# Kernel tuning notes

Measured on AMD Instinct MI355X. Metric: run time of the kernel, lower is better.

## Reference

```python
import jax, jax.numpy as jnp
import numpy as np

B, T, D, ACT, H = 4096, 128, 64, 2, 64

def setup_inputs() -> dict:
    key = jax.random.key(0)
    ks = jax.random.split(key, 8)
    s = 1.0 / np.sqrt(H)
    return {
        "s0": jax.random.normal(ks[0], (B, D), jnp.float32),
        "a": jax.random.normal(ks[1], (B, T, ACT), jnp.float32),
        "w_ih": jax.random.uniform(ks[2], (3 * H, D + ACT), jnp.float32, -s, s),
        "w_hh": jax.random.uniform(ks[3], (3 * H, H), jnp.float32, -s, s),
        "b_ih": jax.random.uniform(ks[4], (3 * H,), jnp.float32, -s, s),
        "b_hh": jax.random.uniform(ks[5], (3 * H,), jnp.float32, -s, s),
        "w_out": jax.random.uniform(ks[6], (D, H), jnp.float32, -s, s),
        "b_out": jax.random.uniform(ks[7], (D,), jnp.float32, -s, s),
    }

def reference(s0, a, w_ih, w_hh, b_ih, b_hh, w_out, b_out):
    # PyTorch GRUCell convention: gates ordered (r, z, n)
    h0 = jnp.zeros((s0.shape[0], w_hh.shape[1]), s0.dtype)

    def step(carry, a_t):
        h, s = carry
        x = jnp.concatenate([s, a_t], axis=-1)              # [B, D+ACT]
        gi = x @ w_ih.T + b_ih                              # [B, 3H]
        gh = h @ w_hh.T + b_hh                              # [B, 3H]
        i_r, i_z, i_n = jnp.split(gi, 3, axis=-1)
        h_r, h_z, h_n = jnp.split(gh, 3, axis=-1)
        r = jax.nn.sigmoid(i_r + h_r)
        z = jax.nn.sigmoid(i_z + h_z)
        n = jnp.tanh(i_n + r * h_n)
        h_new = (1.0 - z) * n + z * h
        s_new = h_new @ w_out.T + b_out                     # [B, D]
        return (h_new, s_new), s_new

    a_tbd = jnp.swapaxes(a, 0, 1)                           # [T, B, ACT]
    _, outs = jax.lax.scan(step, (h0, s0), a_tbd)           # outs: [T, B, D]
    return jnp.swapaxes(outs, 0, 1)                         # [B, T, D]
```

## Files before the change

### kernel.cpp

```cpp
#include <hip/hip_runtime.h>
#include <hip/hip_bf16.h>

typedef __attribute__((ext_vector_type(8))) short bf16x8;
typedef __attribute__((ext_vector_type(4))) float f32x4;
typedef __attribute__((ext_vector_type(2))) float f32x2;

typedef bf16x8 bf16x8_a __attribute__((may_alias));
typedef f32x4  f32x4_a  __attribute__((may_alias));
typedef f32x2  f32x2_a  __attribute__((may_alias));
typedef unsigned short u16a __attribute__((may_alias));
typedef unsigned int u32;

__device__ __forceinline__ float fexp2(float x) {
  float r; asm("v_exp_f32 %0, %1" : "=v"(r) : "v"(x)); return r;
}
__device__ __forceinline__ float frcp(float x) {
  float r; asm("v_rcp_f32 %0, %1" : "=v"(r) : "v"(x)); return r;
}
__device__ __forceinline__ float sigf(float x) {
  return frcp(1.f + fexp2(x * -1.44269504f));
}
__device__ __forceinline__ float tanhf_(float x) {
  return 1.f - 2.f * frcp(1.f + fexp2(x * 2.88539008f));
}
__device__ __forceinline__ u32 cvtpk(float lo, float hi) {
  u32 r; asm("v_cvt_pk_bf16_f32 %0, %1, %2" : "=v"(r) : "v"(lo), "v"(hi)); return r;
}

#define LDS_WG   0
#define LDS_HB   24576
#define LDS_SIZE 28672

__device__ __forceinline__ void stbf(char* smem, int byteoff, float v) {
  union { __hip_bfloat16 b; unsigned short u; } cv;
  cv.b = __float2bfloat16(v);
  *(u16a*)(smem + byteoff) = cv.u;
}
__device__ __forceinline__ void st16(char* smem, int byteoff, unsigned short v) {
  *(u16a*)(smem + byteoff) = v;
}

__device__ __forceinline__ bf16x8 packf8(const float* v) {
  bf16x8 r;
  #pragma unroll
  for (int j = 0; j < 8; ++j) {
    union { __hip_bfloat16 b; short u; } cv;
    cv.b = __float2bfloat16(v[j]);
    r[j] = cv.u;
  }
  return r;
}

__device__ __forceinline__ void xbar() {
  asm volatile("s_waitcnt lgkmcnt(0)\n\ts_barrier" ::: "memory");
}

__global__ __launch_bounds__(256, 1)
void gru_fused(const float* __restrict__ s0, const float* __restrict__ a,
               const float* __restrict__ w_ih, const float* __restrict__ w_hh,
               const float* __restrict__ b_ih, const float* __restrict__ b_hh,
               const float* __restrict__ w_out, const float* __restrict__ b_out,
               float* __restrict__ out)
{
  __shared__ __align__(16) char smem[LDS_SIZE];
  const int tid = threadIdx.x;
  const int l = tid & 63;
  const int w = tid >> 6;
  const int c = l & 15;
  const int g = l >> 4;
  const int b0 = blockIdx.x * 16;
  const int swzc = (c & 7) << 4;

  for (int idx = tid; idx < 16 * 64; idx += 256) {
    int r = idx >> 6, k = idx & 63;
    stbf(smem, LDS_HB + r * 128 + ((k * 2) ^ ((r & 7) << 4)), s0[(b0 + r) * 64 + k]);
  }

  bf16x8 bwo[4][2];
  #pragma unroll
  for (int i = 0; i < 4; ++i) {
    #pragma unroll
    for (int ks = 0; ks < 2; ++ks) {
      float tv[8];
      #pragma unroll
      for (int j = 0; j < 8; ++j)
        tv[j] = w_out[(ks * 32 + g * 8 + j) * 64 + c + 16 * i];
      bwo[i][ks] = packf8(tv);
    }
  }
  #pragma unroll
  for (int rr = 0; rr < 3; ++rr) {
    int rt = w + 4 * rr;
    bf16x8 wsa[2];
    #pragma unroll
    for (int ks = 0; ks < 2; ++ks) {
      float tv[8];
      #pragma unroll
      for (int u = 0; u < 4; ++u) {
        f32x2 t2 = *(const f32x2_a*)(w_ih + (16 * rt + c) * 66 + ks * 32 + g * 8 + 2 * u);
        tv[2 * u] = t2.x; tv[2 * u + 1] = t2.y;
      }
      wsa[ks] = packf8(tv);
    }
    f32x4 acc[4];
    #pragma unroll
    for (int i = 0; i < 4; ++i) {
      #pragma unroll
      for (int j = 0; j < 4; ++j) {
        int n = 16 * rt + 4 * g + j;
        acc[i][j] = (n < 128) ? w_hh[n * 64 + c + 16 * i] : 0.f;
      }
    }
    #pragma unroll
    for (int i = 0; i < 4; ++i)
      #pragma unroll
      for (int ks = 0; ks < 2; ++ks)
        acc[i] = __builtin_amdgcn_mfma_f32_16x16x32_bf16(wsa[ks], bwo[i][ks], acc[i], 0, 0, 0);
    #pragma unroll
    for (int i = 0; i < 4; ++i)
      #pragma unroll
      for (int j = 0; j < 4; ++j) {
        int n = 16 * rt + 4 * g + j;
        stbf(smem, LDS_WG + n * 128 + (((c + 16 * i) * 2) ^ ((n & 7) << 4)), acc[i][j]);
      }
  }

  const int nr = 16 * w + c, nz = 64 + nr, ni = 128 + nr;
  float bs_r = 0.f, bs_z = 0.f, bs_i = 0.f;
  for (int d = 0; d < 64; ++d) {
    float bo = b_out[d];
    bs_r += w_ih[nr * 66 + d] * bo;
    bs_z += w_ih[nz * 66 + d] * bo;
    bs_i += w_ih[ni * 66 + d] * bo;
  }
  const float wa0_r = w_ih[nr * 66 + 64], wa1_r = w_ih[nr * 66 + 65];
  const float wa0_z = w_ih[nz * 66 + 64], wa1_z = w_ih[nz * 66 + 65];
  const float wa0_i = w_ih[ni * 66 + 64], wa1_i = w_ih[ni * 66 + 65];
  const float pb_r = b_ih[nr] + b_hh[nr];
  const float pb_z = b_ih[nz] + b_hh[nz];
  const float pb_i = b_ih[ni];
  const float bias_r = pb_r + bs_r;
  const float bias_z = pb_z + bs_z;
  const float bias_i = pb_i + bs_i;
  const float bias_hn = b_hh[ni];
  const float bias_o = b_out[nr];

  bf16x8 whn[2], wo[2], wsr[2], wsz[2], wsi[2];
  #pragma unroll
  for (int ks = 0; ks < 2; ++ks) {
    float tv[8];
    f32x4 t4;
    t4 = *(const f32x4_a*)(w_hh + ni * 64 + ks * 32 + g * 8);
    tv[0] = t4.x; tv[1] = t4.y; tv[2] = t4.z; tv[3] = t4.w;
    t4 = *(const f32x4_a*)(w_hh + ni * 64 + ks * 32 + g * 8 + 4);
    tv[4] = t4.x; tv[5] = t4.y; tv[6] = t4.z; tv[7] = t4.w;
    whn[ks] = packf8(tv);
    t4 = *(const f32x4_a*)(w_out + nr * 64 + ks * 32 + g * 8);
    tv[0] = t4.x; tv[1] = t4.y; tv[2] = t4.z; tv[3] = t4.w;
    t4 = *(const f32x4_a*)(w_out + nr * 64 + ks * 32 + g * 8 + 4);
    tv[4] = t4.x; tv[5] = t4.y; tv[6] = t4.z; tv[7] = t4.w;
    wo[ks] = packf8(tv);
    #pragma unroll
    for (int u = 0; u < 4; ++u) {
      f32x2 t2 = *(const f32x2_a*)(w_ih + nr * 66 + ks * 32 + g * 8 + 2 * u);
      tv[2 * u] = t2.x; tv[2 * u + 1] = t2.y;
    }
    wsr[ks] = packf8(tv);
    #pragma unroll
    for (int u = 0; u < 4; ++u) {
      f32x2 t2 = *(const f32x2_a*)(w_ih + nz * 66 + ks * 32 + g * 8 + 2 * u);
      tv[2 * u] = t2.x; tv[2 * u + 1] = t2.y;
    }
    wsz[ks] = packf8(tv);
    #pragma unroll
    for (int u = 0; u < 4; ++u) {
      f32x2 t2 = *(const f32x2_a*)(w_ih + ni * 66 + ks * 32 + g * 8 + 2 * u);
      tv[2 * u] = t2.x; tv[2 * u + 1] = t2.y;
    }
    wsi[ks] = packf8(tv);
  }

  __syncthreads();

  bf16x8 wgr[2], wgz[2], wgi[2];
  #pragma unroll
  for (int ks = 0; ks < 2; ++ks) {
    wgr[ks] = *(const bf16x8_a*)(smem + LDS_WG + nr * 128 + ((ks * 64 + g * 16) ^ swzc));
    wgz[ks] = *(const bf16x8_a*)(smem + LDS_WG + nz * 128 + ((ks * 64 + g * 16) ^ swzc));
    wgi[ks] = *(const bf16x8_a*)(smem + LDS_WG + ni * 128 + ((ks * 64 + g * 16) ^ swzc));
  }

  bf16x8 sa[2];
  #pragma unroll
  for (int ks = 0; ks < 2; ++ks)
    sa[ks] = *(const bf16x8_a*)(smem + LDS_HB + c * 128 + ((ks * 64 + g * 16) ^ swzc));
  float a0c[4], a1c[4];
  #pragma unroll
  for (int j = 0; j < 4; ++j) {
    f32x2 av = *(const f32x2_a*)(a + (size_t)(b0 + 4 * g + j) * 256);
    a0c[j] = av.x; a1c[j] = av.y;
  }
  f32x4 ar, az, ai;
  #pragma unroll
  for (int j = 0; j < 4; ++j) {
    ar[j] = pb_r + a0c[j] * wa0_r + a1c[j] * wa1_r;
    az[j] = pb_z + a0c[j] * wa0_z + a1c[j] * wa1_z;
    ai[j] = pb_i + a0c[j] * wa0_i + a1c[j] * wa1_i;
  }
  #pragma unroll
  for (int ks = 0; ks < 2; ++ks) {
    ar = __builtin_amdgcn_mfma_f32_16x16x32_bf16(sa[ks], wsr[ks], ar, 0, 0, 0);
    az = __builtin_amdgcn_mfma_f32_16x16x32_bf16(sa[ks], wsz[ks], az, 0, 0, 0);
    ai = __builtin_amdgcn_mfma_f32_16x16x32_bf16(sa[ks], wsi[ks], ai, 0, 0, 0);
  }
  float hreg[4];
  #pragma unroll
  for (int j = 0; j < 4; ++j) {
    float r = sigf(ar[j]);
    float z = sigf(az[j]);
    float nn = tanhf_(ai[j] + r * bias_hn);
    hreg[j] = nn - z * nn;
  }
  {
    u32 p01 = cvtpk(hreg[0], hreg[1]);
    u32 p23 = cvtpk(hreg[2], hreg[3]);
    int r0 = 4 * g;
    st16(smem, LDS_HB + 2048 + (r0    ) * 128 + ((2 * nr) ^ (((r0    ) & 7) << 4)), (unsigned short)(p01));
    st16(smem, LDS_HB + 2048 + (r0 + 1) * 128 + ((2 * nr) ^ (((r0 + 1) & 7) << 4)), (unsigned short)(p01 >> 16));
    st16(smem, LDS_HB + 2048 + (r0 + 2) * 128 + ((2 * nr) ^ (((r0 + 2) & 7) << 4)), (unsigned short)(p23));
    st16(smem, LDS_HB + 2048 + (r0 + 3) * 128 + ((2 * nr) ^ (((r0 + 3) & 7) << 4)), (unsigned short)(p23 >> 16));
  }
  f32x2 avn[4];
  #pragma unroll
  for (int j = 0; j < 4; ++j)
    avn[j] = *(const f32x2_a*)(a + (size_t)(b0 + 4 * g + j) * 256 + 2);
  xbar();

  #pragma unroll 1
  for (int t = 1; t < 128; ++t) {
    const char* hb = smem + LDS_HB + (t & 1) * 2048 + c * 128;
    bf16x8 ha0 = *(const bf16x8_a*)(hb + ((g * 16) ^ swzc));
    bf16x8 ha1 = *(const bf16x8_a*)(hb + ((64 + g * 16) ^ swzc));

    f32x4 ao = f32x4{bias_o, bias_o, bias_o, bias_o};
    ao = __builtin_amdgcn_mfma_f32_16x16x32_bf16(ha0, wo[0], ao, 0, 0, 0);
    ao = __builtin_amdgcn_mfma_f32_16x16x32_bf16(ha1, wo[1], ao, 0, 0, 0);

    #pragma unroll
    for (int j = 0; j < 4; ++j) { a0c[j] = avn[j].x; a1c[j] = avn[j].y; }
    int tn = (t < 127) ? t + 1 : 127;
    #pragma unroll
    for (int j = 0; j < 4; ++j)
      avn[j] = *(const f32x2_a*)(a + (size_t)(b0 + 4 * g + j) * 256 + 2 * tn);

    f32x4 arr, azz, aii, ahh;
    #pragma unroll
    for (int j = 0; j < 4; ++j) {
      arr[j] = bias_r + a0c[j] * wa0_r + a1c[j] * wa1_r;
      azz[j] = bias_z + a0c[j] * wa0_z + a1c[j] * wa1_z;
      aii[j] = bias_i + a0c[j] * wa0_i + a1c[j] * wa1_i;
      ahh[j] = bias_hn;
    }
    arr = __builtin_amdgcn_mfma_f32_16x16x32_bf16(ha0, wgr[0], arr, 0, 0, 0);
    arr = __builtin_amdgcn_mfma_f32_16x16x32_bf16(ha1, wgr[1], arr, 0, 0, 0);
    azz = __builtin_amdgcn_mfma_f32_16x16x32_bf16(ha0, wgz[0], azz, 0, 0, 0);
    azz = __builtin_amdgcn_mfma_f32_16x16x32_bf16(ha1, wgz[1], azz, 0, 0, 0);
    aii = __builtin_amdgcn_mfma_f32_16x16x32_bf16(ha0, wgi[0], aii, 0, 0, 0);
    aii = __builtin_amdgcn_mfma_f32_16x16x32_bf16(ha1, wgi[1], aii, 0, 0, 0);
    ahh = __builtin_amdgcn_mfma_f32_16x16x32_bf16(ha0, whn[0], ahh, 0, 0, 0);
    ahh = __builtin_amdgcn_mfma_f32_16x16x32_bf16(ha1, whn[1], ahh, 0, 0, 0);

    float hv[4];
    #pragma unroll
    for (int j = 0; j < 4; ++j) {
      float r = sigf(arr[j]);
      float z = sigf(azz[j]);
      float nn = tanhf_(aii[j] + r * ahh[j]);
      float h = nn + z * (hreg[j] - nn);
      hv[j] = h;
      hreg[j] = h;
      out[((size_t)(b0 + 4 * g + j) * 128 + (t - 1)) * 64 + nr] = ao[j];
    }
    {
      u32 p01 = cvtpk(hv[0], hv[1]);
      u32 p23 = cvtpk(hv[2], hv[3]);
      int r0 = 4 * g;
      char* hbn = smem + LDS_HB + ((t + 1) & 1) * 2048;
      st16(hbn, (r0    ) * 128 + ((2 * nr) ^ (((r0    ) & 7) << 4)), (unsigned short)(p01));
      st16(hbn, (r0 + 1) * 128 + ((2 * nr) ^ (((r0 + 1) & 7) << 4)), (unsigned short)(p01 >> 16));
      st16(hbn, (r0 + 2) * 128 + ((2 * nr) ^ (((r0 + 2) & 7) << 4)), (unsigned short)(p23));
      st16(hbn, (r0 + 3) * 128 + ((2 * nr) ^ (((r0 + 3) & 7) << 4)), (unsigned short)(p23 >> 16));
    }
    xbar();
  }

  {
    const char* hb = smem + LDS_HB + 0 * 2048 + c * 128;
    bf16x8 ha0 = *(const bf16x8_a*)(hb + ((g * 16) ^ swzc));
    bf16x8 ha1 = *(const bf16x8_a*)(hb + ((64 + g * 16) ^ swzc));
    f32x4 ao = f32x4{bias_o, bias_o, bias_o, bias_o};
    ao = __builtin_amdgcn_mfma_f32_16x16x32_bf16(ha0, wo[0], ao, 0, 0, 0);
    ao = __builtin_amdgcn_mfma_f32_16x16x32_bf16(ha1, wo[1], ao, 0, 0, 0);
    #pragma unroll
    for (int j = 0; j < 4; ++j)
      out[((size_t)(b0 + 4 * g + j) * 128 + 127) * 64 + nr] = ao[j];
  }
}

extern "C" void kernel_launch(void* const* d_in, const int* in_sizes, int n_in,
                              void* d_out, int out_size, void* d_ws, size_t ws_size,
                              hipStream_t stream) {
  const float* s0    = (const float*)d_in[0];
  const float* a     = (const float*)d_in[1];
  const float* w_ih  = (const float*)d_in[2];
  const float* w_hh  = (const float*)d_in[3];
  const float* b_ih  = (const float*)d_in[4];
  const float* b_hh  = (const float*)d_in[5];
  const float* w_out = (const float*)d_in[6];
  const float* b_out = (const float*)d_in[7];
  float* out = (float*)d_out;
  hipLaunchKernelGGL(gru_fused, dim3(4096 / 16), dim3(256), 0, stream,
                     s0, a, w_ih, w_hh, b_ih, b_hh, w_out, b_out, out);
}
```

Before: 77.92 us.

## Halve batch rows per block to double grid size, padding MFMA tiles

Each block now handles 8 batch rows instead of 16, so the grid grows to 512 blocks and covers more of the CUs on the device. The 16-row MFMA tile is kept, with the unused rows zero-filled, and only lanes with g<2 load inputs and store outputs. Address arithmetic is strength-reduced into incrementing per-row pointers. Half of each MFMA's work is wasted on padding, and the weights are loaded and set up once per block, so the total setup cost doubles.

Result: slower. 125.9 us (+61.6%).

```diff
diff --git a/kernel.cpp b/kernel.cpp
--- a/kernel.cpp
+++ b/kernel.cpp
@@ -68,12 +68,13 @@
   const int w = tid >> 6;
   const int c = l & 15;
   const int g = l >> 4;
-  const int b0 = blockIdx.x * 16;
+  const int b0 = blockIdx.x * 8;
   const int swzc = (c & 7) << 4;
 
   for (int idx = tid; idx < 16 * 64; idx += 256) {
     int r = idx >> 6, k = idx & 63;
-    stbf(smem, LDS_HB + r * 128 + ((k * 2) ^ ((r & 7) << 4)), s0[(b0 + r) * 64 + k]);
+    float v = (r < 8) ? s0[(b0 + r) * 64 + k] : 0.f;
+    stbf(smem, LDS_HB + r * 128 + ((k * 2) ^ ((r & 7) << 4)), v);
   }
 
   bf16x8 bwo[4][2];
@@ -180,6 +181,16 @@
     wsi[ks] = packf8(tv);
   }
 
+  const float* ap[4];
+  float* op[4];
+  #pragma unroll
+  for (int j = 0; j < 4; ++j) {
+    int gr = b0 + 4 * g + j;
+    if (gr > 4095) gr = 4095;
+    ap[j] = a + (size_t)gr * 256;
+    op[j] = out + (size_t)gr * 8192 + nr;
+  }
+
   __syncthreads();
 
   bf16x8 wgr[2], wgz[2], wgi[2];
@@ -197,7 +208,7 @@
   float a0c[4], a1c[4];
   #pragma unroll
   for (int j = 0; j < 4; ++j) {
-    f32x2 av = *(const f32x2_a*)(a + (size_t)(b0 + 4 * g + j) * 256);
+    f32x2 av = *(const f32x2_a*)ap[j];
     a0c[j] = av.x; a1c[j] = av.y;
   }
   f32x4 ar, az, ai;
@@ -232,8 +243,10 @@
   }
   f32x2 avn[4];
   #pragma unroll
-  for (int j = 0; j < 4; ++j)
-    avn[j] = *(const f32x2_a*)(a + (size_t)(b0 + 4 * g + j) * 256 + 2);
+  for (int j = 0; j < 4; ++j) {
+    avn[j] = *(const f32x2_a*)(ap[j] + 2);
+    ap[j] += 4;
+  }
   xbar();
 
   #pragma unroll 1
@@ -248,10 +261,14 @@
 
     #pragma unroll
     for (int j = 0; j < 4; ++j) { a0c[j] = avn[j].x; a1c[j] = avn[j].y; }
-    int tn = (t < 127) ? t + 1 : 127;
+    if (g < 2) {
+      #pragma unroll
+      for (int j = 0; j < 4; ++j)
+        avn[j] = *(const f32x2_a*)ap[j];
+    }
     #pragma unroll
     for (int j = 0; j < 4; ++j)
-      avn[j] = *(const f32x2_a*)(a + (size_t)(b0 + 4 * g + j) * 256 + 2 * tn);
+      ap[j] += (t < 126) ? 2 : 0;
 
     f32x4 arr, azz, aii, ahh;
     #pragma unroll
@@ -279,8 +296,15 @@
       float h = nn + z * (hreg[j] - nn);
       hv[j] = h;
       hreg[j] = h;
-      out[((size_t)(b0 + 4 * g + j) * 128 + (t - 1)) * 64 + nr] = ao[j];
-    }
+    }
+    if (g < 2) {
+      #pragma unroll
+      for (int j = 0; j < 4; ++j)
+        *op[j] = ao[j];
+    }
+    #pragma unroll
+    for (int j = 0; j < 4; ++j)
+      op[j] += 64;
     {
       u32 p01 = cvtpk(hv[0], hv[1]);
       u32 p23 = cvtpk(hv[2], hv[3]);
@@ -301,9 +325,11 @@
     f32x4 ao = f32x4{bias_o, bias_o, bias_o, bias_o};
     ao = __builtin_amdgcn_mfma_f32_16x16x32_bf16(ha0, wo[0], ao, 0, 0, 0);
     ao = __builtin_amdgcn_mfma_f32_16x16x32_bf16(ha1, wo[1], ao, 0, 0, 0);
-    #pragma unroll
-    for (int j = 0; j < 4; ++j)
-      out[((size_t)(b0 + 4 * g + j) * 128 + 127) * 64 + nr] = ao[j];
+    if (g < 2) {
+      #pragma unroll
+      for (int j = 0; j < 4; ++j)
+        *op[j] = ao[j];
+    }
   }
 }
 
@@ -319,6 +345,6 @@
   const float* w_out = (const float*)d_in[6];
   const float* b_out = (const float*)d_in[7];
   float* out = (float*)d_out;
-  hipLaunchKernelGGL(gru_fused, dim3(4096 / 16), dim3(256), 0, stream,
+  hipLaunchKernelGGL(gru_fused, dim3(4096 / 8), dim3(256), 0, stream,
                      s0, a, w_ih, w_hh, b_ih, b_hh, w_out, b_out, out);
 }
```
